# Kernel optimization log

Measured on AMD Instinct MI355X. Metric: run time of the kernel, lower is better.

The kernel has to match this reference:

```python
import jax, jax.numpy as jnp
import numpy as np

B, SEQ, ENC = 128, 1024, 64
D, SEG = 512, 64
SNX = SEQ // SEG   # 16 encoder segments
PRED = 512
SNY = PRED // SEG  # 8 decoder segments


def setup_inputs() -> dict:
    key = jax.random.key(0)
    ks = jax.random.split(key, 18)
    s = 0.05
    r = lambda k, shape: jax.random.normal(k, shape, jnp.float32) * s
    return {
        "x": jax.random.normal(ks[0], (B, SEQ, ENC), jnp.float32),
        # valueEmbedding: Linear(seg_len -> d_model) + SiLU
        "W_emb": r(ks[1], (D, SEG)), "b_emb": r(ks[2], (D,)),
        # GRUCell (encoder residual path)
        "cell_Wih": r(ks[3], (3 * D, D)), "cell_Whh": r(ks[4], (3 * D, D)),
        "cell_bih": r(ks[5], (3 * D,)), "cell_bhh": r(ks[6], (3 * D,)),
        # nn.GRU (decoder, single layer, single step)
        "gru_Wih": r(ks[7], (3 * D, D)), "gru_Whh": r(ks[8], (3 * D, D)),
        "gru_bih": r(ks[9], (3 * D,)), "gru_bhh": r(ks[10], (3 * D,)),
        # residual_projection: Linear(d_model -> d_model)
        "res_W": r(ks[11], (D, D)), "res_b": r(ks[12], (D,)),
        # positional / channel embeddings (each hidden//2)
        "pos_emb": jax.random.normal(ks[13], (SNY, D // 2), jnp.float32),
        "channel_emb": jax.random.normal(ks[14], (ENC, D // 2), jnp.float32),
        # predict: Linear(d_model -> seg_len)
        "pred_W": r(ks[15], (SEG, D)), "pred_b": r(ks[16], (SEG,)),
    }


def gru_step(x_t, h, Wih, Whh, bih, bhh):
    """Single torch-convention GRU step. x_t,h: (N,D)."""
    gx = x_t @ Wih.T + bih          # (N, 3D)
    gh = h @ Whh.T + bhh            # (N, 3D)
    xr, xz, xn = jnp.split(gx, 3, axis=-1)
    hr, hz, hn = jnp.split(gh, 3, axis=-1)
    rg = jax.nn.sigmoid(xr + hr)
    zg = jax.nn.sigmoid(xz + hz)
    ng = jnp.tanh(xn + rg * hn)
    return (1.0 - zg) * ng + zg * h


def reference(x, W_emb, b_emb, cell_Wih, cell_Whh, cell_bih, cell_bhh,
              gru_Wih, gru_Whh, gru_bih, gru_bhh, res_W, res_b,
              pos_emb, channel_emb, pred_W, pred_b):
    seq_last = jax.lax.stop_gradient(x[:, -1:, :])          # (B,1,ENC)
    xs = (x - seq_last).transpose(0, 2, 1).reshape(-1, SNX, SEG)  # (B*ENC, SNX, SEG)
    emb = jax.nn.silu(xs @ W_emb.T + b_emb)                 # (N, SNX, D)
    N = emb.shape[0]

    def step(h, x_t):
        h_cell = gru_step(x_t, h, cell_Wih, cell_Whh, cell_bih, cell_bhh)
        h_new = x_t + (h_cell @ res_W.T + res_b)            # residual projection
        return h_new, None

    h0 = jnp.zeros((N, D), emb.dtype)
    hn, _ = jax.lax.scan(step, h0, jnp.swapaxes(emb, 0, 1))  # hn: (N, D)

    # decoder inputs: [pos_emb | channel_emb] laid out (ENC, SNY, D), tiled over batch
    half = D // 2
    pe = jnp.concatenate([
        jnp.broadcast_to(pos_emb[None, :, :], (ENC, SNY, half)),
        jnp.broadcast_to(channel_emb[:, None, :], (ENC, SNY, half)),
    ], axis=-1).reshape(-1, D)                               # (ENC*SNY, D)
    pe = jnp.tile(pe, (B, 1))                                # (B*ENC*SNY, D)
    h0d = jnp.repeat(hn, SNY, axis=0)                        # (B*ENC*SNY, D)

    hy = gru_step(pe, h0d, gru_Wih, gru_Whh, gru_bih, gru_bhh)  # 1-step GRU decode
    y = hy @ pred_W.T + pred_b                               # (B*ENC*SNY, SEG)
    y = y.reshape(B, ENC, PRED).transpose(0, 2, 1)           # (B, PRED, ENC)
    return y + seq_last
```

## Files before the change

kernel.cpp:

```cpp
#include <hip/hip_runtime.h>
#include <stdint.h>

#define DEV __device__ __forceinline__

typedef __bf16 bf16x8 __attribute__((ext_vector_type(8)));
typedef float  f32x4  __attribute__((ext_vector_type(4)));


DEV unsigned short f2bf(float f){
  union { float f; uint32_t u; } v; v.f = f;
  uint32_t r = (v.u + 0x7FFFu + ((v.u >> 16) & 1u)) >> 16;
  return (unsigned short)r;
}
DEV float bf2f(unsigned short s){
  union { uint32_t u; float f; } v; v.u = ((uint32_t)s) << 16; return v.f;
}
DEV float sigm(float x){
  return __builtin_amdgcn_rcpf(1.0f + __builtin_amdgcn_exp2f(-1.442695041f*x));
}
DEV float tanhe(float x){
  return 1.0f - 2.0f*__builtin_amdgcn_rcpf(__builtin_amdgcn_exp2f(2.885390082f*x) + 1.0f);
}

#define AS1(p) ((const __attribute__((address_space(1))) uint32_t*)(p))
#define AS3(p) ((__attribute__((address_space(3))) uint32_t*)(p))

template<int NROWS, int NW>
DEV void gstage(const unsigned short* src, int ld, unsigned short* lds, int tid){
  constexpr int CH = NROWS/8;
  constexpr int PW = CH/NW;
  int wid = tid >> 6, lane = tid & 63;
  int rsub = lane >> 3;
  int slot = (lane & 7) ^ rsub;
  #pragma unroll
  for (int r = 0; r < PW; r++){
    int chunk = wid*PW + r;
    int row = chunk*8 + rsub;
    __builtin_amdgcn_global_load_lds(AS1(src + (size_t)row*ld + slot*8),
                                     AS3(lds + chunk*512), 16, 0, 0);
  }
}

DEV void zero24(f32x4 (&a)[2][4]){
  f32x4 z = {0.f,0.f,0.f,0.f};
  #pragma unroll
  for (int m = 0; m < 2; m++)
    #pragma unroll
    for (int n = 0; n < 4; n++) a[m][n] = z;
}
DEV void zero22(f32x4 (&a)[2][2]){
  f32x4 z = {0.f,0.f,0.f,0.f};
  #pragma unroll
  for (int m = 0; m < 2; m++)
    #pragma unroll
    for (int n = 0; n < 2; n++) a[m][n] = z;
}

DEV void mmaW(const unsigned short* As, const unsigned short* Bs, int wm0,
              int lane, f32x4 (&acc)[2][4]){
  int lr = lane & 15, lk = (lane >> 4)*8, sw = (lane & 7) << 3;
  #pragma unroll
  for (int ks = 0; ks < 2; ks++){
    int ko = (ks*32 + lk) ^ sw;
    bf16x8 a[2], b[4];
    #pragma unroll
    for (int m = 0; m < 2; m++)
      a[m] = *reinterpret_cast<const bf16x8*>(&As[(wm0 + m*16 + lr)*64 + ko]);
    #pragma unroll
    for (int n = 0; n < 4; n++)
      b[n] = *reinterpret_cast<const bf16x8*>(&Bs[(n*16 + lr)*64 + ko]);
    #pragma unroll
    for (int m = 0; m < 2; m++)
      #pragma unroll
      for (int n = 0; n < 4; n++)
        acc[m][n] = __builtin_amdgcn_mfma_f32_16x16x32_bf16(a[m], b[n], acc[m][n], 0, 0, 0);
  }
}

DEV void mmaW3c(const unsigned short* As, const unsigned short* Bs, int wm0,
                int lane, f32x4 (&a1)[2][2], f32x4 (&a2)[2][2], f32x4 (&a3)[2][2]){
  int lr = lane & 15, lk = (lane >> 4)*8, sw = (lane & 7) << 3;
  #pragma unroll
  for (int ks = 0; ks < 2; ks++){
    int ko = (ks*32 + lk) ^ sw;
    bf16x8 a[2], b[2];
    #pragma unroll
    for (int m = 0; m < 2; m++)
      a[m] = *reinterpret_cast<const bf16x8*>(&As[(wm0 + m*16 + lr)*64 + ko]);
    #pragma unroll
    for (int n = 0; n < 2; n++)
      b[n] = *reinterpret_cast<const bf16x8*>(&Bs[(n*16 + lr)*64 + ko]);
    #pragma unroll
    for (int m = 0; m < 2; m++)
      #pragma unroll
      for (int n = 0; n < 2; n++)
        a1[m][n] = __builtin_amdgcn_mfma_f32_16x16x32_bf16(a[m], b[n], a1[m][n], 0, 0, 0);
    #pragma unroll
    for (int n = 0; n < 2; n++)
      b[n] = *reinterpret_cast<const bf16x8*>(&Bs[2048 + (n*16 + lr)*64 + ko]);
    #pragma unroll
    for (int m = 0; m < 2; m++)
      #pragma unroll
      for (int n = 0; n < 2; n++)
        a2[m][n] = __builtin_amdgcn_mfma_f32_16x16x32_bf16(a[m], b[n], a2[m][n], 0, 0, 0);
    #pragma unroll
    for (int n = 0; n < 2; n++)
      b[n] = *reinterpret_cast<const bf16x8*>(&Bs[4096 + (n*16 + lr)*64 + ko]);
    #pragma unroll
    for (int m = 0; m < 2; m++)
      #pragma unroll
      for (int n = 0; n < 2; n++)
        a3[m][n] = __builtin_amdgcn_mfma_f32_16x16x32_bf16(a[m], b[n], a3[m][n], 0, 0, 0);
  }
}

DEV void kloopS(const unsigned short* A0, const unsigned short* B0,
                unsigned short* As, unsigned short* Bs,
                int tid, int wm0, int lane, f32x4 (&acc)[2][4]){
  for (int kt = 0; kt < 8; kt++){
    gstage<128,4>(A0 + kt*64, 512, As, tid);
    gstage<64,4>(B0 + kt*64, 512, Bs, tid);
    __syncthreads();
    mmaW(As, Bs, wm0, lane, acc);
    __syncthreads();
  }
}

__global__ __launch_bounds__(256) void cvt_all_kernel(
    const float* cWih, const float* cWhh, const float* gWih, const float* gWhh,
    const float* resW, const float* predW, const float* Wemb,
    unsigned short* o0, unsigned short* o1, unsigned short* o2, unsigned short* o3,
    unsigned short* o4, unsigned short* o5, unsigned short* o6){
  int g = blockIdx.x*256 + threadIdx.x;
  const float* s; unsigned short* d; int idx;
  if      (g < 196608){ s=cWih;  d=o0; idx=g; }
  else if (g < 393216){ s=cWhh;  d=o1; idx=g-196608; }
  else if (g < 589824){ s=gWih;  d=o2; idx=g-393216; }
  else if (g < 786432){ s=gWhh;  d=o3; idx=g-589824; }
  else if (g < 851968){ s=resW;  d=o4; idx=g-786432; }
  else if (g < 860160){ s=predW; d=o5; idx=g-851968; }
  else if (g < 868352){ s=Wemb;  d=o6; idx=g-860160; }
  else return;
  float4 v = reinterpret_cast<const float4*>(s)[idx];
  ushort4 r; r.x=f2bf(v.x); r.y=f2bf(v.y); r.z=f2bf(v.z); r.w=f2bf(v.w);
  reinterpret_cast<ushort4*>(d)[idx] = r;
}

__global__ __launch_bounds__(256) void build_pe_kernel(const float* pos, const float* chan, unsigned short* pe){
  int i = blockIdx.x*256 + threadIdx.x;
  if (i >= 512*512) return;
  int m = i >> 9, d = i & 511;
  int c = m >> 3, sy = m & 7;
  float v = (d < 256) ? pos[sy*256 + d] : chan[c*256 + (d-256)];
  pe[i] = f2bf(v);
}

__global__ __launch_bounds__(256) void xs_kernel(const float* __restrict__ x,
                                                 unsigned short* __restrict__ xs){
  __shared__ float tile[64][65];
  __shared__ float lastv[64];
  int b = blockIdx.y, tk0 = blockIdx.x*64, tid = threadIdx.x;
  if (tid < 64) lastv[tid] = x[(size_t)b*65536 + 65472 + tid];
  #pragma unroll
  for (int k = 0; k < 16; k++){
    int id = tid + k*256;
    int i = id >> 6, c = id & 63;
    tile[i][c] = x[(size_t)b*65536 + (size_t)(tk0+i)*64 + c];
  }
  __syncthreads();
  #pragma unroll
  for (int k = 0; k < 16; k++){
    int id = tid + k*256;
    int c = id >> 6, i = id & 63;
    xs[(size_t)(b*64 + c)*1024 + tk0 + i] = f2bf(tile[i][c] - lastv[c]);
  }
}

__global__ __launch_bounds__(256) void embed_kernel(const unsigned short* __restrict__ xs,
    const unsigned short* __restrict__ wemb, const float* __restrict__ bemb,
    unsigned short* __restrict__ embout, int t0, size_t zs){
  __shared__ unsigned short As[8192];
  __shared__ unsigned short Bs[4096];
  int tid = threadIdx.x, lane = tid & 63, wid = tid >> 6, wm0 = wid*32;
  int rA0 = blockIdx.x*128, d0 = blockIdx.y*64;
  int t = t0 + blockIdx.z;
  unsigned short* out = embout + (size_t)blockIdx.z * zs;

  gstage<128,4>(xs + (size_t)rA0*1024 + t*64, 1024, As, tid);
  gstage<64,4>(wemb + (size_t)d0*64, 64, Bs, tid);
  __syncthreads();
  f32x4 acc[2][4]; zero24(acc);
  mmaW(As, Bs, wm0, lane, acc);

  int lr = lane & 15, lj = (lane >> 4)*4;
  #pragma unroll
  for (int m = 0; m < 2; m++)
    #pragma unroll
    for (int n = 0; n < 4; n++){
      int col = d0 + n*16 + lr;
      float bb = bemb[col];
      #pragma unroll
      for (int j = 0; j < 4; j++){
        int row = rA0 + wm0 + m*16 + lj + j;
        float v = acc[m][n][j] + bb;
        v = v * sigm(v);
        out[(size_t)row*512 + col] = f2bf(v);
      }
    }
}

__global__ __launch_bounds__(256,4) void gates_kernel(
    const unsigned short* __restrict__ emb, const unsigned short* __restrict__ hbf,
    const unsigned short* __restrict__ Wih, const unsigned short* __restrict__ Whh,
    const float* __restrict__ bih, const float* __restrict__ bhh,
    unsigned short* __restrict__ hcell){
  __shared__ unsigned short As[8192];
  __shared__ unsigned short Bs[3*2048];
  int tid = threadIdx.x, lane = tid & 63, wid = tid >> 6, wm0 = wid*32;
  int id = blockIdx.x;
  int g = (id & 7) + ((id >> 7) << 3);
  int c = (id >> 3) & 15;
  int rA0 = g*128, d0 = c*32;

  f32x4 aR[2][2], aZ[2][2], aNx[2][2], aNh[2][2];
  zero22(aR); zero22(aZ); zero22(aNx); zero22(aNh);

  {
    const unsigned short* A = emb + (size_t)rA0*512;
    const unsigned short* BR = Wih + (size_t)d0*512;
    const unsigned short* BZ = Wih + (size_t)(512 + d0)*512;
    const unsigned short* BN = Wih + (size_t)(1024 + d0)*512;
    for (int kt = 0; kt < 8; kt++){
      gstage<128,4>(A + kt*64, 512, As, tid);
      gstage<32,4>(BR + kt*64, 512, Bs, tid);
      gstage<32,4>(BZ + kt*64, 512, Bs + 2048, tid);
      gstage<32,4>(BN + kt*64, 512, Bs + 4096, tid);
      __syncthreads();
      mmaW3c(As, Bs, wm0, lane, aR, aZ, aNx);
      __syncthreads();
    }
  }
  {
    const unsigned short* A = hbf + (size_t)rA0*512;
    const unsigned short* BR = Whh + (size_t)d0*512;
    const unsigned short* BZ = Whh + (size_t)(512 + d0)*512;
    const unsigned short* BN = Whh + (size_t)(1024 + d0)*512;
    for (int kt = 0; kt < 8; kt++){
      gstage<128,4>(A + kt*64, 512, As, tid);
      gstage<32,4>(BR + kt*64, 512, Bs, tid);
      gstage<32,4>(BZ + kt*64, 512, Bs + 2048, tid);
      gstage<32,4>(BN + kt*64, 512, Bs + 4096, tid);
      __syncthreads();
      mmaW3c(As, Bs, wm0, lane, aR, aZ, aNh);
      __syncthreads();
    }
  }

  int lr = lane & 15, lj = (lane >> 4)*4;
  #pragma unroll
  for (int n = 0; n < 2; n++){
    int col = d0 + n*16 + lr;
    float brr = bih[col] + bhh[col];
    float bzz = bih[512 + col] + bhh[512 + col];
    float bni = bih[1024 + col], bnh = bhh[1024 + col];
    #pragma unroll
    for (int m = 0; m < 2; m++)
      #pragma unroll
      for (int j = 0; j < 4; j++){
        int row = rA0 + wm0 + m*16 + lj + j;
        float rg = sigm(aR[m][n][j] + brr);
        float zg = sigm(aZ[m][n][j] + bzz);
        float ng = tanhe(aNx[m][n][j] + bni + rg*(aNh[m][n][j] + bnh));
        float h  = bf2f(hbf[(size_t)row*512 + col]);
        hcell[(size_t)row*512 + col] = f2bf((1.0f - zg)*ng + zg*h);
      }
  }
}

__global__ __launch_bounds__(256) void res_kernel(
    const unsigned short* __restrict__ hcell, const unsigned short* __restrict__ Wres,
    const float* __restrict__ res_b, const unsigned short* __restrict__ emb,
    unsigned short* __restrict__ hbf){
  __shared__ unsigned short As[8192];
  __shared__ unsigned short Bs[4096];
  int tid = threadIdx.x, lane = tid & 63, wid = tid >> 6, wm0 = wid*32;
  int rA0 = blockIdx.x*128, d0 = blockIdx.y*64;

  f32x4 acc[2][4]; zero24(acc);
  kloopS(hcell + (size_t)rA0*512, Wres + (size_t)d0*512, As, Bs, tid, wm0, lane, acc);

  int lr = lane & 15, lj = (lane >> 4)*4;
  #pragma unroll
  for (int m = 0; m < 2; m++)
    #pragma unroll
    for (int n = 0; n < 4; n++){
      int col = d0 + n*16 + lr;
      float bb = res_b[col];
      #pragma unroll
      for (int j = 0; j < 4; j++){
        int row = rA0 + wm0 + m*16 + lj + j;
        float v = acc[m][n][j] + bb + bf2f(emb[(size_t)row*512 + col]);
        hbf[(size_t)row*512 + col] = f2bf(v);
      }
    }
}

template<bool BF16OUT>
__global__ __launch_bounds__(256) void gemm_bias_kernel(
    const unsigned short* __restrict__ A, const unsigned short* __restrict__ B,
    const float* __restrict__ bias, float* __restrict__ Cf,
    unsigned short* __restrict__ Cb, int Nld){
  __shared__ unsigned short As[8192];
  __shared__ unsigned short Bs[4096];
  int tid = threadIdx.x, lane = tid & 63, wid = tid >> 6, wm0 = wid*32;
  int rA0 = blockIdx.x*128, rB0 = blockIdx.y*64;

  f32x4 acc[2][4]; zero24(acc);
  kloopS(A + (size_t)rA0*512, B + (size_t)rB0*512, As, Bs, tid, wm0, lane, acc);

  int lr = lane & 15, lj = (lane >> 4)*4;
  #pragma unroll
  for (int m = 0; m < 2; m++)
    #pragma unroll
    for (int n = 0; n < 4; n++){
      int col = rB0 + n*16 + lr;
      float bb = bias[col];
      #pragma unroll
      for (int j = 0; j < 4; j++){
        int row = rA0 + wm0 + m*16 + lj + j;
        float v = acc[m][n][j] + bb;
        if (BF16OUT) Cb[(size_t)row*Nld + col] = f2bf(v);
        else         Cf[(size_t)row*Nld + col] = v;
      }
    }
}

DEV void bf8ld(const unsigned short* p, float* o){
  uint4 u = *reinterpret_cast<const uint4*>(p);
  union { uint32_t w; float f; } v;
  v.w = u.x << 16;          o[0] = v.f;
  v.w = u.x & 0xffff0000u;  o[1] = v.f;
  v.w = u.y << 16;          o[2] = v.f;
  v.w = u.y & 0xffff0000u;  o[3] = v.f;
  v.w = u.z << 16;          o[4] = v.f;
  v.w = u.z & 0xffff0000u;  o[5] = v.f;
  v.w = u.w << 16;          o[6] = v.f;
  v.w = u.w & 0xffff0000u;  o[7] = v.f;
}

__global__ __launch_bounds__(256) void hy_kernel(const unsigned short* __restrict__ gxd,
    const unsigned short* __restrict__ ghd, const unsigned short* __restrict__ hb,
    unsigned short* __restrict__ hy){
  int gid = blockIdx.x*256 + threadIdx.x;
  #pragma unroll 1
  for (int it = 0; it < 8; it++, gid += 2048*256){
    int r = gid >> 6, dg = gid & 63;
    int n = r >> 3, sy = r & 7, c = n & 63, mpe = c*8 + sy;
    int d = dg*8;
    const unsigned short* gx = gxd + (size_t)mpe*1536 + d;
    const unsigned short* gh = ghd + (size_t)n*1536 + d;
    const unsigned short* hh = hb + (size_t)n*512 + d;
    float xr[8], xz[8], xn[8], hr[8], hz[8], hn[8], h[8];
    bf8ld(gx, xr); bf8ld(gx + 512, xz); bf8ld(gx + 1024, xn);
    bf8ld(gh, hr); bf8ld(gh + 512, hz); bf8ld(gh + 1024, hn); bf8ld(hh, h);
    unsigned short w[8];
    #pragma unroll
    for (int j = 0; j < 8; j++){
      float rg = sigm(xr[j] + hr[j]);
      float zg = sigm(xz[j] + hz[j]);
      float ng = tanhe(xn[j] + rg*hn[j]);
      w[j] = f2bf((1.0f - zg)*ng + zg*h[j]);
    }
    *reinterpret_cast<uint4*>(hy + (size_t)r*512 + d) =
        *reinterpret_cast<const uint4*>(w);
  }
}

__global__ __launch_bounds__(256) void pred_kernel(
    const unsigned short* __restrict__ hy, const unsigned short* __restrict__ predW,
    const float* __restrict__ predb, const float* __restrict__ x,
    float* __restrict__ out){
  __shared__ unsigned short As[8192];
  __shared__ unsigned short Bs[4096];
  int tid = threadIdx.x, lane = tid & 63, wid = tid >> 6, wm0 = wid*32;
  int rA0 = blockIdx.x*128;

  f32x4 acc[2][4]; zero24(acc);
  kloopS(hy + (size_t)rA0*512, predW, As, Bs, tid, wm0, lane, acc);

  int lr = lane & 15, lj = (lane >> 4)*4;
  #pragma unroll
  for (int n = 0; n < 4; n++){
    int s = n*16 + lr;
    float bb = predb[s];
    #pragma unroll
    for (int m = 0; m < 2; m++)
      #pragma unroll
      for (int j = 0; j < 4; j++){
        int r = rA0 + wm0 + m*16 + lj + j;
        int nn = r >> 3, sy = r & 7, b = nn >> 6, c = nn & 63;
        out[(size_t)b*32768 + (size_t)(sy*64 + s)*64 + c] =
            acc[m][n][j] + bb + x[(size_t)b*65536 + 65472 + c];
      }
  }
}

extern "C" void kernel_launch(void* const* d_in, const int* in_sizes, int n_in,
                              void* d_out, int out_size, void* d_ws, size_t ws_size,
                              hipStream_t stream){
  (void)in_sizes; (void)n_in; (void)out_size;
  const float* x     = (const float*)d_in[0];
  const float* Wemb  = (const float*)d_in[1];
  const float* bemb  = (const float*)d_in[2];
  const float* cWih  = (const float*)d_in[3];
  const float* cWhh  = (const float*)d_in[4];
  const float* cbih  = (const float*)d_in[5];
  const float* cbhh  = (const float*)d_in[6];
  const float* gWih  = (const float*)d_in[7];
  const float* gWhh  = (const float*)d_in[8];
  const float* gbih  = (const float*)d_in[9];
  const float* gbhh  = (const float*)d_in[10];
  const float* resW  = (const float*)d_in[11];
  const float* resb  = (const float*)d_in[12];
  const float* pos   = (const float*)d_in[13];
  const float* chan  = (const float*)d_in[14];
  const float* predW = (const float*)d_in[15];
  const float* predb = (const float*)d_in[16];
  float* out = (float*)d_out;

  uint8_t* ws = (uint8_t*)d_ws;
  size_t o = 0;
  auto take = [&](size_t bytes){ uint8_t* p = ws + o; o += (bytes + 255) & ~(size_t)255; return p; };
  unsigned short* wb_cWih  = (unsigned short*)take(786432*2);
  unsigned short* wb_cWhh  = (unsigned short*)take(786432*2);
  unsigned short* wb_gWih  = (unsigned short*)take(786432*2);
  unsigned short* wb_gWhh  = (unsigned short*)take(786432*2);
  unsigned short* wb_resW  = (unsigned short*)take(262144*2);
  unsigned short* wb_predW = (unsigned short*)take(32768*2);
  unsigned short* wb_Wemb  = (unsigned short*)take(32768*2);
  unsigned short* pe_bf    = (unsigned short*)take(262144*2);
  unsigned short* h_bf     = (unsigned short*)take(4194304*2);

  uint8_t* U = ws + o;
  unsigned short* xs_all = (unsigned short*)(U);
  unsigned short* hcell  = (unsigned short*)(U + 16777216);
  unsigned short* emb    = (unsigned short*)(U + 25165824);
  unsigned short* ghd    = (unsigned short*)(U);
  unsigned short* gxd    = (unsigned short*)(U + 25165824);
  unsigned short* hy     = (unsigned short*)(U + 28311552);

  bool big = ws_size >= o + (size_t)25165824 + (size_t)16*8388608;
  size_t zs = big ? 4194304 : 0;

  cvt_all_kernel<<<3392, 256, 0, stream>>>(cWih, cWhh, gWih, gWhh, resW, predW, Wemb,
      wb_cWih, wb_cWhh, wb_gWih, wb_gWhh, wb_resW, wb_predW, wb_Wemb);
  build_pe_kernel<<<1024, 256, 0, stream>>>(pos, chan, pe_bf);
  xs_kernel<<<dim3(16, 128), 256, 0, stream>>>(x, xs_all);
  hipMemsetAsync(h_bf, 0, (size_t)4194304*2, stream);

  if (big)
    embed_kernel<<<dim3(64, 8, 16), 256, 0, stream>>>(xs_all, wb_Wemb, bemb, emb, 0, zs);

  for (int t = 0; t < 16; t++){
    const unsigned short* emb_t = emb + (big ? (size_t)t*4194304 : 0);
    if (!big)
      embed_kernel<<<dim3(64, 8, 1), 256, 0, stream>>>(xs_all, wb_Wemb, bemb,
                                                       (unsigned short*)emb_t, t, 0);
    gates_kernel<<<1024, 256, 0, stream>>>(emb_t, h_bf, wb_cWih, wb_cWhh,
                                           cbih, cbhh, hcell);
    res_kernel<<<dim3(64, 8), 256, 0, stream>>>(hcell, wb_resW, resb, emb_t, h_bf);
  }

  gemm_bias_kernel<true><<<dim3(64, 24), 256, 0, stream>>>(h_bf, wb_gWhh, gbhh,
                                                           nullptr, ghd, 1536);
  gemm_bias_kernel<true><<<dim3(4, 24), 256, 0, stream>>>(pe_bf, wb_gWih, gbih,
                                                          nullptr, gxd, 1536);
  hy_kernel<<<2048, 256, 0, stream>>>(gxd, ghd, h_bf, hy);
  pred_kernel<<<512, 256, 0, stream>>>(hy, wb_predW, predb, x, out);
}
```

Baseline: 748.2 us.

## Shrink res_kernel tiles to 64x64 with grouped block ordering and more blocks

The residual projection GEMM now uses 64x64 output tiles with a 2x2 warp layout instead of 128x64, launching 1024 one-dimensional blocks rather than 512. Block indices are remapped so that groups of 8 row tiles share a column tile, which should improve L2 reuse of the weight and activation tiles. The kernel uses an inline K-loop with swizzled LDS reads and launch bounds of 4 blocks per SM to raise occupancy on the 256-CU device, in exchange for less register-level reuse per tile.

```diff
diff --git a/kernel.cpp b/kernel.cpp
--- a/kernel.cpp
+++ b/kernel.cpp
@@ -277,32 +277,60 @@
   }
 }
 
-__global__ __launch_bounds__(256) void res_kernel(
+__global__ __launch_bounds__(256,4) void res_kernel(
     const unsigned short* __restrict__ hcell, const unsigned short* __restrict__ Wres,
     const float* __restrict__ res_b, const unsigned short* __restrict__ emb,
     unsigned short* __restrict__ hbf){
-  __shared__ unsigned short As[8192];
+  __shared__ unsigned short As[4096];
   __shared__ unsigned short Bs[4096];
-  int tid = threadIdx.x, lane = tid & 63, wid = tid >> 6, wm0 = wid*32;
-  int rA0 = blockIdx.x*128, d0 = blockIdx.y*64;
-
-  f32x4 acc[2][4]; zero24(acc);
-  kloopS(hcell + (size_t)rA0*512, Wres + (size_t)d0*512, As, Bs, tid, wm0, lane, acc);
-
-  int lr = lane & 15, lj = (lane >> 4)*4;
-  #pragma unroll
-  for (int m = 0; m < 2; m++)
-    #pragma unroll
-    for (int n = 0; n < 4; n++){
-      int col = d0 + n*16 + lr;
-      float bb = res_b[col];
+  int tid = threadIdx.x, lane = tid & 63, wid = tid >> 6;
+  int wm0 = (wid >> 1)*32, wn0 = (wid & 1)*32;
+  int id = blockIdx.x;
+  int g = (id & 7) + ((id >> 6) << 3);
+  int c = (id >> 3) & 7;
+  int rA0 = g*64, d0 = c*64;
+
+  f32x4 acc[2][2]; zero22(acc);
+  const unsigned short* A = hcell + (size_t)rA0*512;
+  const unsigned short* Bw = Wres + (size_t)d0*512;
+  int lr = lane & 15, lk = (lane >> 4)*8, sw = (lane & 7) << 3;
+  for (int kt = 0; kt < 8; kt++){
+    gstage<64,4>(A + kt*64, 512, As, tid);
+    gstage<64,4>(Bw + kt*64, 512, Bs, tid);
+    __syncthreads();
+    #pragma unroll
+    for (int ks = 0; ks < 2; ks++){
+      int ko = (ks*32 + lk) ^ sw;
+      bf16x8 a[2], b[2];
+      #pragma unroll
+      for (int m = 0; m < 2; m++)
+        a[m] = *reinterpret_cast<const bf16x8*>(&As[(wm0 + m*16 + lr)*64 + ko]);
+      #pragma unroll
+      for (int n = 0; n < 2; n++)
+        b[n] = *reinterpret_cast<const bf16x8*>(&Bs[(wn0 + n*16 + lr)*64 + ko]);
+      #pragma unroll
+      for (int m = 0; m < 2; m++)
+        #pragma unroll
+        for (int n = 0; n < 2; n++)
+          acc[m][n] = __builtin_amdgcn_mfma_f32_16x16x32_bf16(a[m], b[n], acc[m][n], 0, 0, 0);
+    }
+    __syncthreads();
+  }
+
+  int lj = (lane >> 4)*4;
+  #pragma unroll
+  for (int n = 0; n < 2; n++){
+    int col = d0 + wn0 + n*16 + lr;
+    float bb = res_b[col];
+    #pragma unroll
+    for (int m = 0; m < 2; m++)
       #pragma unroll
       for (int j = 0; j < 4; j++){
         int row = rA0 + wm0 + m*16 + lj + j;
         float v = acc[m][n][j] + bb + bf2f(emb[(size_t)row*512 + col]);
         hbf[(size_t)row*512 + col] = f2bf(v);
       }
-    }
+  }
 }
 
 template<bool BF16OUT>
@@ -468,7 +496,7 @@
                                                        (unsigned short*)emb_t, t, 0);
     gates_kernel<<<1024, 256, 0, stream>>>(emb_t, h_bf, wb_cWih, wb_cWhh,
                                            cbih, cbhh, hcell);
-    res_kernel<<<dim3(64, 8), 256, 0, stream>>>(hcell, wb_resW, resb, emb_t, h_bf);
+    res_kernel<<<1024, 256, 0, stream>>>(hcell, wb_resW, resb, emb_t, h_bf);
   }
 
   gemm_bias_kernel<true><<<dim3(64, 24), 256, 0, stream>>>(h_bf, wb_gWhh, gbhh,
```

Measured after the change: 749.6 us. No clear change (+0.2%).
